# Kernel optimization log

Hardware: AMD Instinct MI355X
Metric: run time of the kernel (lower is better)

Reference implementation:

```python
import jax, jax.numpy as jnp
import numpy as np

NTOKENS = 50257
NHID = 1024
TPC = int(np.ceil(np.sqrt(NTOKENS)))          # 225 tokens per class
NCLASSES = int(np.ceil(NTOKENS / TPC))        # 224 classes
BATCH = 2048
INITRANGE = 0.1


def setup_inputs() -> dict:
    key = jax.random.key(0)
    k1, k2, k3, k4 = jax.random.split(key, 4)
    inputs = jax.random.normal(k1, (BATCH, NHID), dtype=jnp.float32)
    labels = jax.random.randint(k2, (BATCH,), 0, NTOKENS, dtype=jnp.int32)
    W_top = jax.random.uniform(k3, (NHID, NCLASSES), dtype=jnp.float32,
                               minval=-INITRANGE, maxval=INITRANGE)
    b_top = jnp.zeros((NCLASSES,), dtype=jnp.float32)
    W_bottom = jax.random.uniform(k4, (NCLASSES, NHID, TPC), dtype=jnp.float32,
                                  minval=-INITRANGE, maxval=INITRANGE)
    b_bottom = jnp.zeros((NCLASSES, TPC), dtype=jnp.float32)
    return {"inputs": inputs, "labels": labels, "W_top": W_top, "b_top": b_top,
            "W_bottom": W_bottom, "b_bottom": b_bottom}


def reference(inputs, labels, W_top, b_top, W_bottom, b_bottom):
    # Two-level hierarchical softmax: P(word) = P(class | h) * P(word | class, h)
    batch = inputs.shape[0]
    cls = labels // TPC          # [B] class index at top level
    word = labels % TPC          # [B] word index within class

    # Top level: [B, nclasses]
    top_probs = jax.nn.softmax(inputs @ W_top + b_top, axis=1)
    p_cls = top_probs[jnp.arange(batch), cls]            # [B]

    # Bottom level: gather per-example class weights then batched matvec
    Wb = W_bottom[cls]                                    # [B, nhid, tpc]
    bb = b_bottom[cls]                                    # [B, tpc]
    bottom_logits = jnp.einsum('bd,bdk->bk', inputs, Wb) + bb
    bottom_probs = jax.nn.softmax(bottom_logits, axis=1)
    p_word = bottom_probs[jnp.arange(batch), word]        # [B]

    return p_cls * p_word
```

## Files before the change

kernel.cpp:

```cpp
#include <hip/hip_runtime.h>
#include <math.h>

#define TPC 225
#define NCLS 224
#define NHID 1024
#define BATCH 2048
#define CAP 256
#define LSTRIDE 256

__global__ __launch_bounds__(256) void hs_bucket(const int* __restrict__ labels,
                                                 int* __restrict__ bucket,
                                                 int* __restrict__ cnt) {
    __shared__ int scnt[NCLS];
    const int t = threadIdx.x;
    for (int i = t; i < NCLS; i += 256) scnt[i] = 0;
    __syncthreads();
    for (int b = t; b < BATCH; b += 256) {
        int lab = labels[b];
        int c = lab / TPC;
        int pos = atomicAdd(&scnt[c], 1);
        bucket[c * CAP + pos] = b;
    }
    __syncthreads();
    for (int i = t; i < NCLS; i += 256) cnt[i] = scnt[i];
}

__global__ __launch_bounds__(1024, 4) void hs_tlogits(const float* __restrict__ x,
                                                      const float* __restrict__ W,
                                                      float* __restrict__ tws) {
    __shared__ float red[8 * 8 * 256];
    const int t = threadIdx.x;
    const int lane = t & 63;
    const int wave = t >> 6;
    const int wr = wave & 1;
    const int wd = wave >> 1;
    const int r0 = blockIdx.x * 8;

    const float* pj[4];
#pragma unroll
    for (int j = 0; j < 4; j++) {
        int k = 64 * j + lane;
        pj[j] = W + (size_t)wd * 128 * NCLS + (k < NCLS ? k : NCLS - 1);
    }
    const float* xp[4];
#pragma unroll
    for (int rl = 0; rl < 4; rl++)
        xp[rl] = x + (size_t)(r0 + wr * 4 + rl) * NHID + wd * 128;

    float acc[4][4] = {};
    for (int dq = 0; dq < 32; ++dq) {
        float w[4][4];
#pragma unroll
        for (int di = 0; di < 4; di++)
#pragma unroll
            for (int j = 0; j < 4; j++) w[di][j] = pj[j][di * NCLS];
#pragma unroll
        for (int rl = 0; rl < 4; rl++) {
            float4 xq = *(const float4*)(xp[rl] + dq * 4);
#pragma unroll
            for (int di = 0; di < 4; di++) {
                float xv = ((const float*)&xq)[di];
#pragma unroll
                for (int j = 0; j < 4; j++)
                    acc[rl][j] = fmaf(xv, w[di][j], acc[rl][j]);
            }
        }
#pragma unroll
        for (int j = 0; j < 4; j++) pj[j] += 4 * NCLS;
    }
#pragma unroll
    for (int rl = 0; rl < 4; rl++)
#pragma unroll
        for (int j = 0; j < 4; j++)
            red[(wd * 8 + wr * 4 + rl) * 256 + 64 * j + lane] = acc[rl][j];
    __syncthreads();

    const int u = t & 255;
    for (int r = t >> 8; r < 8; r += 4) {
        if (u < NCLS) {
            float s = 0.f;
#pragma unroll
            for (int w8 = 0; w8 < 8; w8++) s += red[(w8 * 8 + r) * 256 + u];
            tws[(size_t)(r0 + r) * LSTRIDE + u] = s;
        }
    }
}

#define LOADW(W)                                              \
    do {                                                      \
        _Pragma("unroll") for (int di = 0; di < 4; di++)      \
            _Pragma("unroll") for (int j = 0; j < 4; j++)     \
                W[di][j] = pj[j][di * TPC];                   \
        _Pragma("unroll") for (int j = 0; j < 4; j++)         \
            pj[j] += 4 * TPC;                                 \
    } while (0)

#define LOADX(X, dq)                                          \
    do {                                                      \
        _Pragma("unroll") for (int rl = 0; rl < RW; rl++)     \
            X[rl] = *(const float4*)(xp[rl] + (dq) * 4);      \
    } while (0)

#define FMAS(W, X)                                            \
    do {                                                      \
        _Pragma("unroll") for (int rl = 0; rl < RW; rl++) {   \
            _Pragma("unroll") for (int di = 0; di < 4; di++) {\
                float xv = ((const float*)&X[rl])[di];        \
                _Pragma("unroll") for (int j = 0; j < 4; j++) \
                    acc[rl][j] = fmaf(xv, W[di][j], acc[rl][j]); \
            }                                                 \
        }                                                     \
    } while (0)

template <int RW>
__device__ __forceinline__ void bpass4(const float* __restrict__ xq,
                                       const float* __restrict__ wq,
                                       const int* __restrict__ bucket_c,
                                       const int base, const int n,
                                       const int lane, const int wr,
                                       float* __restrict__ bp) {
    const float* xp[RW];
    int rows[RW];
#pragma unroll
    for (int rl = 0; rl < RW; rl++) {
        int idx = base + wr * RW + rl;
        int row = bucket_c[idx < n ? idx : 0];
        rows[rl] = (idx < n) ? row : -1;
        xp[rl] = xq + (size_t)row * NHID;
    }
    const float* pj[4];
#pragma unroll
    for (int j = 0; j < 4; j++) {
        int k = 64 * j + lane;
        pj[j] = wq + (k < TPC ? k : TPC - 1);
    }
    float acc[RW][4] = {};
    float wA[4][4], wB[4][4];
    float4 xA[RW], xB[RW];

    LOADW(wA);
    LOADX(xA, 0);
    for (int dq = 0; dq < 64; dq += 2) {
        LOADW(wB);
        LOADX(xB, dq + 1);
        FMAS(wA, xA);
        if (dq + 2 < 64) {
            LOADW(wA);
            LOADX(xA, dq + 2);
        }
        FMAS(wB, xB);
    }

#pragma unroll
    for (int rl = 0; rl < RW; rl++) {
        if (rows[rl] >= 0) {
#pragma unroll
            for (int j = 0; j < 4; j++) {
                int k = 64 * j + lane;
                if (k < TPC) bp[(size_t)rows[rl] * LSTRIDE + k] = acc[rl][j];
            }
        }
    }
}

__global__ __launch_bounds__(256, 4) void hs_blogits(const float* __restrict__ x,
                                                     const float* __restrict__ Wb,
                                                     const int* __restrict__ bucket,
                                                     const int* __restrict__ cnt,
                                                     float* __restrict__ bws) {
    const int c = blockIdx.x >> 2;
    const int q = blockIdx.x & 3;
    const int n = cnt[c];
    if (n == 0) return;
    const int lane = threadIdx.x & 63;
    const int wr = threadIdx.x >> 6;
    const float* wq = Wb + (size_t)c * (NHID * TPC) + (size_t)q * 256 * TPC;
    const float* xq = x + q * 256;
    const int* bucket_c = bucket + c * CAP;
    float* bp = bws + (size_t)q * BATCH * LSTRIDE;

    for (int base = 0; base < n; base += 16) {
        int m = n - base;
        if (m > 16) m = 16;
        const int RW = (m + 3) >> 2;
        switch (RW) {
            case 1: bpass4<1>(xq, wq, bucket_c, base, n, lane, wr, bp); break;
            case 2: bpass4<2>(xq, wq, bucket_c, base, n, lane, wr, bp); break;
            case 3: bpass4<3>(xq, wq, bucket_c, base, n, lane, wr, bp); break;
            default: bpass4<4>(xq, wq, bucket_c, base, n, lane, wr, bp); break;
        }
    }
}

__global__ __launch_bounds__(256) void hs_finish(const float* __restrict__ tws,
                                                 const float* __restrict__ bws,
                                                 const int* __restrict__ labels,
                                                 const float* __restrict__ b_top,
                                                 const float* __restrict__ b_bot,
                                                 float* __restrict__ out) {
    const int lane = threadIdx.x & 63;
    const int wave = threadIdx.x >> 6;
    const int row = blockIdx.x * 4 + wave;
    const int label = labels[row];
    const int c = label / TPC;
    const int word = label - c * TPC;

    float p[2];
#pragma unroll
    for (int lvl = 0; lvl < 2; lvl++) {
        const int NS = lvl ? TPC : NCLS;
        const int pick = lvl ? word : c;
        const float* bias = lvl ? (b_bot + c * TPC) : b_top;
        float lg[4];
#pragma unroll
        for (int j = 0; j < 4; j++) {
            int k = lane + 64 * j;
            if (k < NS) {
                float v;
                if (lvl == 0) {
                    v = tws[(size_t)row * LSTRIDE + k];
                } else {
                    v = bws[(size_t)row * LSTRIDE + k]
                      + bws[(size_t)(BATCH + row) * LSTRIDE + k]
                      + bws[(size_t)(2 * BATCH + row) * LSTRIDE + k]
                      + bws[(size_t)(3 * BATCH + row) * LSTRIDE + k];
                }
                lg[j] = v + bias[k];
            } else {
                lg[j] = -INFINITY;
            }
        }
        float m = fmaxf(fmaxf(lg[0], lg[1]), fmaxf(lg[2], lg[3]));
#pragma unroll
        for (int off = 32; off > 0; off >>= 1) m = fmaxf(m, __shfl_xor(m, off, 64));
        float s = 0.f, pp = 0.f;
#pragma unroll
        for (int j = 0; j < 4; j++) {
            int k = lane + 64 * j;
            float e = (k < NS) ? __expf(lg[j] - m) : 0.f;
            s += e;
            if (k == pick) pp = e;
        }
#pragma unroll
        for (int off = 32; off > 0; off >>= 1) {
            s += __shfl_xor(s, off, 64);
            pp += __shfl_xor(pp, off, 64);
        }
        p[lvl] = pp / s;
    }
    if (lane == 0) out[row] = p[0] * p[1];
}

extern "C" void kernel_launch(void* const* d_in, const int* in_sizes, int n_in,
                              void* d_out, int out_size, void* d_ws, size_t ws_size,
                              hipStream_t stream) {
    const float* inputs   = (const float*)d_in[0];
    const int*   labels   = (const int*)d_in[1];
    const float* W_top    = (const float*)d_in[2];
    const float* b_top    = (const float*)d_in[3];
    const float* W_bottom = (const float*)d_in[4];
    const float* b_bottom = (const float*)d_in[5];
    float* out = (float*)d_out;

    int* bucket = (int*)d_ws;
    int* cnt    = bucket + NCLS * CAP;
    float* tws  = (float*)(cnt + NCLS);
    float* bws  = tws + (size_t)BATCH * LSTRIDE;

    hs_bucket<<<1, 256, 0, stream>>>(labels, bucket, cnt);
    hs_tlogits<<<256, 1024, 0, stream>>>(inputs, W_top, tws);
    hs_blogits<<<NCLS * 4, 256, 0, stream>>>(inputs, W_bottom, bucket, cnt, bws);
    hs_finish<<<BATCH / 4, 256, 0, stream>>>(tws, bws, labels, b_top, b_bottom, out);
}
```

Baseline: 416.8 us.

## Split hidden dimension into 8 chunks for both logit GEMMs with partial-sum workspace

The top-level logits kernel loses its shared-memory reduction. It becomes a split-K kernel over 8 hidden-dimension chunks that writes per-chunk partial logits, reusing a shared double-buffered gemm_chunk helper. The bottom-level kernel also moves from 4 to 8 hidden chunks, which doubles the block count, and its occupancy hint rises. The finish kernel now sums 8 partial slices for each level. The aim is more parallelism and latency hiding across the GPU, paid for with more workspace traffic and extra reads in the finish kernel.

Result: slower. 1.533 ms (+267.8%).

```diff
diff --git a/kernel.cpp b/kernel.cpp
--- a/kernel.cpp
+++ b/kernel.cpp
@@ -7,6 +7,9 @@
 #define BATCH 2048
 #define CAP 256
 #define LSTRIDE 256
+#define NCHUNK 8
+#define CHUNK_D 128
+#define NDQ 32
 
 __global__ __launch_bounds__(256) void hs_bucket(const int* __restrict__ labels,
                                                  int* __restrict__ bucket,
@@ -25,74 +28,13 @@
     for (int i = t; i < NCLS; i += 256) cnt[i] = scnt[i];
 }
 
-__global__ __launch_bounds__(1024, 4) void hs_tlogits(const float* __restrict__ x,
-                                                      const float* __restrict__ W,
-                                                      float* __restrict__ tws) {
-    __shared__ float red[8 * 8 * 256];
-    const int t = threadIdx.x;
-    const int lane = t & 63;
-    const int wave = t >> 6;
-    const int wr = wave & 1;
-    const int wd = wave >> 1;
-    const int r0 = blockIdx.x * 8;
-
-    const float* pj[4];
-#pragma unroll
-    for (int j = 0; j < 4; j++) {
-        int k = 64 * j + lane;
-        pj[j] = W + (size_t)wd * 128 * NCLS + (k < NCLS ? k : NCLS - 1);
-    }
-    const float* xp[4];
-#pragma unroll
-    for (int rl = 0; rl < 4; rl++)
-        xp[rl] = x + (size_t)(r0 + wr * 4 + rl) * NHID + wd * 128;
-
-    float acc[4][4] = {};
-    for (int dq = 0; dq < 32; ++dq) {
-        float w[4][4];
-#pragma unroll
-        for (int di = 0; di < 4; di++)
-#pragma unroll
-            for (int j = 0; j < 4; j++) w[di][j] = pj[j][di * NCLS];
-#pragma unroll
-        for (int rl = 0; rl < 4; rl++) {
-            float4 xq = *(const float4*)(xp[rl] + dq * 4);
-#pragma unroll
-            for (int di = 0; di < 4; di++) {
-                float xv = ((const float*)&xq)[di];
-#pragma unroll
-                for (int j = 0; j < 4; j++)
-                    acc[rl][j] = fmaf(xv, w[di][j], acc[rl][j]);
-            }
-        }
-#pragma unroll
-        for (int j = 0; j < 4; j++) pj[j] += 4 * NCLS;
-    }
-#pragma unroll
-    for (int rl = 0; rl < 4; rl++)
-#pragma unroll
-        for (int j = 0; j < 4; j++)
-            red[(wd * 8 + wr * 4 + rl) * 256 + 64 * j + lane] = acc[rl][j];
-    __syncthreads();
-
-    const int u = t & 255;
-    for (int r = t >> 8; r < 8; r += 4) {
-        if (u < NCLS) {
-            float s = 0.f;
-#pragma unroll
-            for (int w8 = 0; w8 < 8; w8++) s += red[(w8 * 8 + r) * 256 + u];
-            tws[(size_t)(r0 + r) * LSTRIDE + u] = s;
-        }
-    }
-}
-
 #define LOADW(W)                                              \
     do {                                                      \
         _Pragma("unroll") for (int di = 0; di < 4; di++)      \
             _Pragma("unroll") for (int j = 0; j < 4; j++)     \
-                W[di][j] = pj[j][di * TPC];                   \
+                W[di][j] = pj[j][di * KS];                    \
         _Pragma("unroll") for (int j = 0; j < 4; j++)         \
-            pj[j] += 4 * TPC;                                 \
+            pj[j] += 4 * KS;                                  \
     } while (0)
 
 #define LOADX(X, dq)                                          \
@@ -112,48 +54,83 @@
         }                                                     \
     } while (0)
 
+template <int RW, int KS>
+__device__ __forceinline__ void gemm_chunk(const float* __restrict__ xb,
+                                           const int* rows,
+                                           const float* __restrict__ wq,
+                                           const int lane,
+                                           float acc[RW][4]) {
+    const float* xp[RW];
+#pragma unroll
+    for (int rl = 0; rl < RW; rl++) xp[rl] = xb + (size_t)rows[rl] * NHID;
+    const float* pj[4];
+#pragma unroll
+    for (int j = 0; j < 4; j++) {
+        int k = 64 * j + lane;
+        pj[j] = wq + (k < KS ? k : KS - 1);
+    }
+#pragma unroll
+    for (int rl = 0; rl < RW; rl++)
+#pragma unroll
+        for (int j = 0; j < 4; j++) acc[rl][j] = 0.f;
+
+    float wA[4][4], wB[4][4];
+    float4 xA[RW], xB[RW];
+    LOADW(wA);
+    LOADX(xA, 0);
+    for (int dq = 0; dq < NDQ; dq += 2) {
+        LOADW(wB);
+        LOADX(xB, dq + 1);
+        FMAS(wA, xA);
+        if (dq + 2 < NDQ) {
+            LOADW(wA);
+            LOADX(xA, dq + 2);
+        }
+        FMAS(wB, xB);
+    }
+}
+
+__global__ __launch_bounds__(256, 8) void hs_tlogits(const float* __restrict__ x,
+                                                     const float* __restrict__ W,
+                                                     float* __restrict__ twsP) {
+    const int rb = blockIdx.x >> 3;
+    const int q = blockIdx.x & 7;
+    const int lane = threadIdx.x & 63;
+    const int wr = threadIdx.x >> 6;
+    int rows[2] = {rb * 8 + wr * 2, rb * 8 + wr * 2 + 1};
+    const float* xb = x + q * CHUNK_D;
+    const float* wq = W + (size_t)q * CHUNK_D * NCLS;
+    float acc[2][4];
+    gemm_chunk<2, NCLS>(xb, rows, wq, lane, acc);
+    float* tp = twsP + (size_t)q * BATCH * LSTRIDE;
+#pragma unroll
+    for (int rl = 0; rl < 2; rl++)
+#pragma unroll
+        for (int j = 0; j < 4; j++) {
+            int k = 64 * j + lane;
+            if (k < NCLS) tp[(size_t)rows[rl] * LSTRIDE + k] = acc[rl][j];
+        }
+}
+
 template <int RW>
-__device__ __forceinline__ void bpass4(const float* __restrict__ xq,
+__device__ __forceinline__ void bchunk(const float* __restrict__ xb,
                                        const float* __restrict__ wq,
                                        const int* __restrict__ bucket_c,
                                        const int base, const int n,
                                        const int lane, const int wr,
                                        float* __restrict__ bp) {
-    const float* xp[RW];
-    int rows[RW];
+    int rows[RW], rval[RW];
 #pragma unroll
     for (int rl = 0; rl < RW; rl++) {
         int idx = base + wr * RW + rl;
-        int row = bucket_c[idx < n ? idx : 0];
-        rows[rl] = (idx < n) ? row : -1;
-        xp[rl] = xq + (size_t)row * NHID;
-    }
-    const float* pj[4];
-#pragma unroll
-    for (int j = 0; j < 4; j++) {
-        int k = 64 * j + lane;
-        pj[j] = wq + (k < TPC ? k : TPC - 1);
-    }
-    float acc[RW][4] = {};
-    float wA[4][4], wB[4][4];
-    float4 xA[RW], xB[RW];
-
-    LOADW(wA);
-    LOADX(xA, 0);
-    for (int dq = 0; dq < 64; dq += 2) {
-        LOADW(wB);
-        LOADX(xB, dq + 1);
-        FMAS(wA, xA);
-        if (dq + 2 < 64) {
-            LOADW(wA);
-            LOADX(xA, dq + 2);
-        }
-        FMAS(wB, xB);
-    }
-
+        rows[rl] = bucket_c[idx < n ? idx : 0];
+        rval[rl] = (idx < n);
+    }
+    float acc[RW][4];
+    gemm_chunk<RW, TPC>(xb, rows, wq, lane, acc);
 #pragma unroll
     for (int rl = 0; rl < RW; rl++) {
-        if (rows[rl] >= 0) {
+        if (rval[rl]) {
 #pragma unroll
             for (int j = 0; j < 4; j++) {
                 int k = 64 * j + lane;
@@ -163,19 +140,19 @@
     }
 }
 
-__global__ __launch_bounds__(256, 4) void hs_blogits(const float* __restrict__ x,
+__global__ __launch_bounds__(256, 7) void hs_blogits(const float* __restrict__ x,
                                                      const float* __restrict__ Wb,
                                                      const int* __restrict__ bucket,
                                                      const int* __restrict__ cnt,
                                                      float* __restrict__ bws) {
-    const int c = blockIdx.x >> 2;
-    const int q = blockIdx.x & 3;
+    const int c = blockIdx.x >> 3;
+    const int q = blockIdx.x & 7;
     const int n = cnt[c];
     if (n == 0) return;
     const int lane = threadIdx.x & 63;
     const int wr = threadIdx.x >> 6;
-    const float* wq = Wb + (size_t)c * (NHID * TPC) + (size_t)q * 256 * TPC;
-    const float* xq = x + q * 256;
+    const float* wq = Wb + (size_t)c * (NHID * TPC) + (size_t)q * CHUNK_D * TPC;
+    const float* xb = x + q * CHUNK_D;
     const int* bucket_c = bucket + c * CAP;
     float* bp = bws + (size_t)q * BATCH * LSTRIDE;
 
@@ -184,10 +161,10 @@
         if (m > 16) m = 16;
         const int RW = (m + 3) >> 2;
         switch (RW) {
-            case 1: bpass4<1>(xq, wq, bucket_c, base, n, lane, wr, bp); break;
-            case 2: bpass4<2>(xq, wq, bucket_c, base, n, lane, wr, bp); break;
-            case 3: bpass4<3>(xq, wq, bucket_c, base, n, lane, wr, bp); break;
-            default: bpass4<4>(xq, wq, bucket_c, base, n, lane, wr, bp); break;
+            case 1: bchunk<1>(xb, wq, bucket_c, base, n, lane, wr, bp); break;
+            case 2: bchunk<2>(xb, wq, bucket_c, base, n, lane, wr, bp); break;
+            case 3: bchunk<3>(xb, wq, bucket_c, base, n, lane, wr, bp); break;
+            default: bchunk<4>(xb, wq, bucket_c, base, n, lane, wr, bp); break;
         }
     }
 }
@@ -210,21 +187,17 @@
     for (int lvl = 0; lvl < 2; lvl++) {
         const int NS = lvl ? TPC : NCLS;
         const int pick = lvl ? word : c;
+        const float* lws = lvl ? bws : tws;
         const float* bias = lvl ? (b_bot + c * TPC) : b_top;
         float lg[4];
 #pragma unroll
         for (int j = 0; j < 4; j++) {
             int k = lane + 64 * j;
             if (k < NS) {
-                float v;
-                if (lvl == 0) {
-                    v = tws[(size_t)row * LSTRIDE + k];
-                } else {
-                    v = bws[(size_t)row * LSTRIDE + k]
-                      + bws[(size_t)(BATCH + row) * LSTRIDE + k]
-                      + bws[(size_t)(2 * BATCH + row) * LSTRIDE + k]
-                      + bws[(size_t)(3 * BATCH + row) * LSTRIDE + k];
-                }
+                float v = 0.f;
+#pragma unroll
+                for (int pq = 0; pq < NCHUNK; pq++)
+                    v += lws[((size_t)pq * BATCH + row) * LSTRIDE + k];
                 lg[j] = v + bias[k];
             } else {
                 lg[j] = -INFINITY;
@@ -265,10 +238,10 @@
     int* bucket = (int*)d_ws;
     int* cnt    = bucket + NCLS * CAP;
     float* tws  = (float*)(cnt + NCLS);
-    float* bws  = tws + (size_t)BATCH * LSTRIDE;
+    float* bws  = tws + (size_t)NCHUNK * BATCH * LSTRIDE;
 
     hs_bucket<<<1, 256, 0, stream>>>(labels, bucket, cnt);
-    hs_tlogits<<<256, 1024, 0, stream>>>(inputs, W_top, tws);
-    hs_blogits<<<NCLS * 4, 256, 0, stream>>>(inputs, W_bottom, bucket, cnt, bws);
+    hs_tlogits<<<256 * NCHUNK, 256, 0, stream>>>(inputs, W_top, tws);
+    hs_blogits<<<NCLS * NCHUNK, 256, 0, stream>>>(inputs, W_bottom, bucket, cnt, bws);
     hs_finish<<<BATCH / 4, 256, 0, stream>>>(tws, bws, labels, b_top, b_bottom, out);
 }
```
